# Performance work log

Hardware: AMD Instinct MI355X
Metric: run time of the kernel (lower is better)

The kernel has to match this reference:

```python
import math
import jax, jax.numpy as jnp
import numpy as np

N, D = 16384, 1024


def setup_inputs() -> dict:
    key = jax.random.key(0)
    k1, k2 = jax.random.split(key)
    return {
        "image_embeddings_aligned": jax.random.normal(k1, (N, D), dtype=jnp.float32),
        "text_embeddings_aligned": jax.random.normal(k2, (N, D), dtype=jnp.float32),
        "logit_scale": jnp.asarray(math.log(20.0), dtype=jnp.float32),  # stored as log(init)
        "logit_bias": jnp.asarray(-10.0, dtype=jnp.float32),
    }


def _l2_normalize(x, eps=1e-12):
    # matches F.normalize(p=2, dim=-1)
    n = jnp.linalg.norm(x, axis=-1, keepdims=True)
    return x / jnp.maximum(n, eps)


def reference(image_embeddings_aligned, text_embeddings_aligned, logit_scale, logit_bias):
    img = _l2_normalize(image_embeddings_aligned)
    txt = _l2_normalize(text_embeddings_aligned)
    # [N, N] pairwise logits
    logits = jnp.exp(logit_scale) * jnp.einsum("nd,md->nm", img, txt) + logit_bias
    n = logits.shape[0]
    labels = 2.0 * jnp.eye(n, dtype=logits.dtype) - 1.0  # +1 on diagonal, -1 off
    loss_matrix = jax.nn.log_sigmoid(labels * logits)
    siglip_loss = -jnp.mean(loss_matrix)  # total_loss (structure_lambda == 0)
    return siglip_loss
```

## Files before the change

### kernel.cpp

```cpp
#include <hip/hip_runtime.h>

#define NROWS 16384
#define DIM   1024
#define QSCALE 32.0f
#define E8M0S  0x7A7A7A7Au

typedef int    v4i    __attribute__((ext_vector_type(4)));
typedef int    v8i    __attribute__((ext_vector_type(8)));
typedef float  f32x16 __attribute__((ext_vector_type(16)));

__device__ __forceinline__ void glds16(const void* g, void* l) {
    __builtin_amdgcn_global_load_lds(
        (const __attribute__((address_space(1))) void*)g,
        (__attribute__((address_space(3))) void*)l,
        16, 0, 0);
}

__device__ __forceinline__ float fexp2(float x) {
#if __has_builtin(__builtin_amdgcn_exp2f)
    return __builtin_amdgcn_exp2f(x);
#else
    return exp2f(x);
#endif
}
__device__ __forceinline__ float flog2(float x) {
#if __has_builtin(__builtin_amdgcn_logf)
    return __builtin_amdgcn_logf(x);
#else
    return log2f(x);
#endif
}

__device__ __forceinline__ unsigned fp4_nib(float y) {
    unsigned s = (__float_as_uint(y) >> 31) << 3;
    float a = fminf(fabsf(y), 6.0f);
    unsigned c = (unsigned)(a >= 0.25f) + (unsigned)(a >= 0.75f) +
                 (unsigned)(a >= 1.25f) + (unsigned)(a >= 1.75f) +
                 (unsigned)(a >= 2.5f)  + (unsigned)(a >= 3.5f)  +
                 (unsigned)(a >= 5.0f);
    return c | s;
}

__global__ __launch_bounds__(256) void norm_fused(
    const float* __restrict__ img,
    const float* __restrict__ txt,
    unsigned char* __restrict__ imgQ,
    unsigned char* __restrict__ txtQ,
    const float* __restrict__ lscale,
    const float* __restrict__ lbias,
    float* __restrict__ diagPart) {
    const int t    = threadIdx.x;
    const int lane = t & 63;
    const int wave = t >> 6;
    const int gw   = blockIdx.x * 4 + wave;
    const float sc   = __expf(lscale[0]);
    const float bias = lbias[0];

    for (int row = gw; row < NROWS; row += 8192) {
        const float4* pi = (const float4*)(img + (size_t)row * DIM);
        const float4* pt = (const float4*)(txt + (size_t)row * DIM);
        float4 vi[4], vt[4];
        float ssi = 0.0f, sst = 0.0f, dot = 0.0f;
        #pragma unroll
        for (int j = 0; j < 4; ++j) {
            vi[j] = pi[lane * 4 + j];
            vt[j] = pt[lane * 4 + j];
            ssi += vi[j].x*vi[j].x + vi[j].y*vi[j].y + vi[j].z*vi[j].z + vi[j].w*vi[j].w;
            sst += vt[j].x*vt[j].x + vt[j].y*vt[j].y + vt[j].z*vt[j].z + vt[j].w*vt[j].w;
            dot += vi[j].x*vt[j].x + vi[j].y*vt[j].y + vi[j].z*vt[j].z + vi[j].w*vt[j].w;
        }
        #pragma unroll
        for (int off = 1; off < 64; off <<= 1) {
            ssi += __shfl_xor(ssi, off, 64);
            sst += __shfl_xor(sst, off, 64);
            dot += __shfl_xor(dot, off, 64);
        }
        const float ii = 1.0f / fmaxf(sqrtf(ssi), 1e-12f);
        const float it = 1.0f / fmaxf(sqrtf(sst), 1e-12f);
        if (lane == 0) diagPart[row] = -fmaf(sc, dot * ii * it, bias);

        const float qi = ii * QSCALE, qt = it * QSCALE;
        uint2 oi, ot;
        {
            const float* fi = (const float*)vi;
            const float* ft = (const float*)vt;
            unsigned lo = 0, hi = 0, lo2 = 0, hi2 = 0;
            #pragma unroll
            for (int e = 0; e < 8; ++e) {
                lo  |= fp4_nib(fi[e]     * qi) << (4 * e);
                hi  |= fp4_nib(fi[e + 8] * qi) << (4 * e);
                lo2 |= fp4_nib(ft[e]     * qt) << (4 * e);
                hi2 |= fp4_nib(ft[e + 8] * qt) << (4 * e);
            }
            oi.x = lo;  oi.y = hi;
            ot.x = lo2; ot.y = hi2;
        }
        ((uint2*)(imgQ + (size_t)row * 512))[lane] = oi;
        ((uint2*)(txtQ + (size_t)row * 512))[lane] = ot;
    }
}

__global__ __launch_bounds__(256) void siglip_gemm(
    const unsigned char* __restrict__ A,
    const unsigned char* __restrict__ B,
    const float* __restrict__ lscale,
    const float* __restrict__ lbias,
    float* __restrict__ gemmPart)
{
    __shared__ unsigned char sA[128 * 128];
    __shared__ unsigned char sB[128 * 128];
    __shared__ float wred[4];

    const int t    = threadIdx.x;
    const int lane = t & 63;
    const int wave = t >> 6;
    const int wr   = wave >> 1;
    const int wc   = wave & 1;
    const int r31  = lane & 31;
    const int h    = lane >> 5;
    const int xr   = (r31 & 7) ^ ((r31 >> 4) & 1);

    const int GRID = NROWS / 128;
    const int GM = 16;
    int b = blockIdx.x;
    int group = b / (GM * GRID);
    int ing   = b % (GM * GRID);
    int brow  = group * GM + (ing % GM);
    int bcol  = ing / GM;

    const size_t aBase = (size_t)brow * 128;
    const size_t bBase = (size_t)bcol * 128;

    const int srow = lane >> 3;
    const int c0   = (lane & 7) ^ srow;
    const int d01  = (c0 & 1) ? -16 : 16;

    const unsigned char* aP = A + (size_t)(aBase + wave * 32 + srow) * 512 + c0 * 16;
    const unsigned char* bP = B + (size_t)(bBase + wave * 32 + srow) * 512 + c0 * 16;
    char* lA0 = ((char*)sA) + wave * 4096;
    char* lB0 = ((char*)sB) + wave * 4096;

    int rbA[2], rbB[2];
    #pragma unroll
    for (int i = 0; i < 2; ++i) {
        rbA[i] = (wr * 64 + i * 32 + r31) * 128;
        rbB[i] = (wc * 64 + i * 32 + r31) * 128;
    }

    f32x16 acc[2][2] = {};

    for (int k = 0; k < 4; ++k) {
        __syncthreads();
        #pragma unroll
        for (int j = 0; j < 4; ++j) {
            const int tog = (j >> 1) ? d01 : 0;
            glds16(aP + j * 4096 + tog, lA0 + j * 1024);
            glds16(bP + j * 4096 + tog, lB0 + j * 1024);
        }
        aP += 128;
        bP += 128;
        __syncthreads();

        #pragma unroll
        for (int ks = 0; ks < 4; ++ks) {
            const int s = ((ks * 2 + h) ^ xr) * 16;
            v4i a0 = *(const v4i*)(sA + rbA[0] + s);
            v4i a1 = *(const v4i*)(sA + rbA[1] + s);
            v4i b0 = *(const v4i*)(sB + rbB[0] + s);
            v4i b1 = *(const v4i*)(sB + rbB[1] + s);
            v8i af[2], bf[2];
            af[0] = __builtin_shufflevector(a0, a0, 0, 1, 2, 3, -1, -1, -1, -1);
            af[1] = __builtin_shufflevector(a1, a1, 0, 1, 2, 3, -1, -1, -1, -1);
            bf[0] = __builtin_shufflevector(b0, b0, 0, 1, 2, 3, -1, -1, -1, -1);
            bf[1] = __builtin_shufflevector(b1, b1, 0, 1, 2, 3, -1, -1, -1, -1);
            #pragma unroll
            for (int mi = 0; mi < 2; ++mi)
                #pragma unroll
                for (int ni = 0; ni < 2; ++ni)
                    acc[mi][ni] = __builtin_amdgcn_mfma_scale_f32_32x32x64_f8f6f4(
                        af[mi], bf[ni], acc[mi][ni],
                        4, 4,
                        0, (int)E8M0S,
                        0, (int)E8M0S);
        }
    }

    const float l2e   = 1.44269504088896341f;
    const float scale = __expf(lscale[0]);
    const float aCo   = scale * l2e;
    const float bCo   = lbias[0] * l2e;
    float local = 0.0f;
    #pragma unroll
    for (int mi = 0; mi < 2; ++mi)
        #pragma unroll
        for (int ni = 0; ni < 2; ++ni)
            #pragma unroll
            for (int r = 0; r < 16; r += 4) {
                float e0 = fexp2(fmaf(aCo, acc[mi][ni][r + 0], bCo));
                float e1 = fexp2(fmaf(aCo, acc[mi][ni][r + 1], bCo));
                float e2 = fexp2(fmaf(aCo, acc[mi][ni][r + 2], bCo));
                float e3 = fexp2(fmaf(aCo, acc[mi][ni][r + 3], bCo));
                float p  = ((1.0f + e0) * (1.0f + e1)) *
                           ((1.0f + e2) * (1.0f + e3));
                local += flog2(p);
            }

    #pragma unroll
    for (int off = 32; off > 0; off >>= 1) local += __shfl_down(local, off, 64);
    if (lane == 0) wred[wave] = local;
    __syncthreads();
    if (t == 0)
        gemmPart[blockIdx.x] =
            (wred[0] + wred[1] + wred[2] + wred[3]) * 0.69314718055994531f;
}

__global__ __launch_bounds__(1024) void finalize_kernel(
    const float* __restrict__ parts, float* __restrict__ out) {
    __shared__ float wr[16];
    const int t    = threadIdx.x;
    const int lane = t & 63;
    const int wave = t >> 6;
    const float4* p4 = (const float4*)parts;
    float s = 0.0f;
    for (int i = t; i < 8192; i += 1024) {
        float4 v = p4[i];
        s += v.x + v.y + v.z + v.w;
    }
    #pragma unroll
    for (int off = 32; off > 0; off >>= 1) s += __shfl_down(s, off, 64);
    if (lane == 0) wr[wave] = s;
    __syncthreads();
    if (t == 0) {
        float tot = 0.0f;
        #pragma unroll
        for (int i = 0; i < 16; ++i) tot += wr[i];
        out[0] = tot / 268435456.0f;
    }
}

extern "C" void kernel_launch(void* const* d_in, const int* in_sizes, int n_in,
                              void* d_out, int out_size, void* d_ws, size_t ws_size,
                              hipStream_t stream) {
    const float* img    = (const float*)d_in[0];
    const float* txt    = (const float*)d_in[1];
    const float* lscale = (const float*)d_in[2];
    const float* lbias  = (const float*)d_in[3];
    float* out = (float*)d_out;

    char* ws = (char*)d_ws;
    unsigned char* imgQ = (unsigned char*)ws;
    unsigned char* txtQ = (unsigned char*)(ws + (size_t)NROWS * 512);
    float* parts   = (float*)(ws + (size_t)2 * NROWS * 512);
    float* diagPart = parts;
    float* gemmPart = parts + NROWS;

    norm_fused<<<2048, 256, 0, stream>>>(img, txt, imgQ, txtQ, lscale, lbias, diagPart);
    siglip_gemm<<<dim3((NROWS / 128) * (NROWS / 128)), 256, 0, stream>>>(
        imgQ, txtQ, lscale, lbias, gemmPart);
    finalize_kernel<<<1, 1024, 0, stream>>>(parts, out);
}
```

Measured before the change: 311.9 us.

## Enlarge GEMM tile to 256x128 and coalesce quantization loads/stores

```diff
diff --git a/kernel.cpp b/kernel.cpp
--- a/kernel.cpp
+++ b/kernel.cpp
@@ -63,8 +63,8 @@
         float ssi = 0.0f, sst = 0.0f, dot = 0.0f;
         #pragma unroll
         for (int j = 0; j < 4; ++j) {
-            vi[j] = pi[lane * 4 + j];
-            vt[j] = pt[lane * 4 + j];
+            vi[j] = pi[lane + 64 * j];
+            vt[j] = pt[lane + 64 * j];
             ssi += vi[j].x*vi[j].x + vi[j].y*vi[j].y + vi[j].z*vi[j].z + vi[j].w*vi[j].w;
             sst += vt[j].x*vt[j].x + vt[j].y*vt[j].y + vt[j].z*vt[j].z + vt[j].w*vt[j].w;
             dot += vi[j].x*vt[j].x + vi[j].y*vt[j].y + vi[j].z*vt[j].z + vi[j].w*vt[j].w;
@@ -80,34 +80,28 @@
         if (lane == 0) diagPart[row] = -fmaf(sc, dot * ii * it, bias);
 
         const float qi = ii * QSCALE, qt = it * QSCALE;
-        uint2 oi, ot;
-        {
-            const float* fi = (const float*)vi;
-            const float* ft = (const float*)vt;
-            unsigned lo = 0, hi = 0, lo2 = 0, hi2 = 0;
-            #pragma unroll
-            for (int e = 0; e < 8; ++e) {
-                lo  |= fp4_nib(fi[e]     * qi) << (4 * e);
-                hi  |= fp4_nib(fi[e + 8] * qi) << (4 * e);
-                lo2 |= fp4_nib(ft[e]     * qt) << (4 * e);
-                hi2 |= fp4_nib(ft[e + 8] * qt) << (4 * e);
-            }
-            oi.x = lo;  oi.y = hi;
-            ot.x = lo2; ot.y = hi2;
-        }
-        ((uint2*)(imgQ + (size_t)row * 512))[lane] = oi;
-        ((uint2*)(txtQ + (size_t)row * 512))[lane] = ot;
-    }
-}
-
-__global__ __launch_bounds__(256) void siglip_gemm(
+        ushort* oi = (ushort*)(imgQ + (size_t)row * 512);
+        ushort* ot = (ushort*)(txtQ + (size_t)row * 512);
+        #pragma unroll
+        for (int j = 0; j < 4; ++j) {
+            unsigned p = fp4_nib(vi[j].x * qi)        | (fp4_nib(vi[j].y * qi) << 4) |
+                         (fp4_nib(vi[j].z * qi) << 8) | (fp4_nib(vi[j].w * qi) << 12);
+            unsigned q = fp4_nib(vt[j].x * qt)        | (fp4_nib(vt[j].y * qt) << 4) |
+                         (fp4_nib(vt[j].z * qt) << 8) | (fp4_nib(vt[j].w * qt) << 12);
+            oi[lane + 64 * j] = (ushort)p;
+            ot[lane + 64 * j] = (ushort)q;
+        }
+    }
+}
+
+__global__ __launch_bounds__(256, 2) void siglip_gemm(
     const unsigned char* __restrict__ A,
     const unsigned char* __restrict__ B,
     const float* __restrict__ lscale,
     const float* __restrict__ lbias,
     float* __restrict__ gemmPart)
 {
-    __shared__ unsigned char sA[128 * 128];
+    __shared__ unsigned char sA[256 * 128];
     __shared__ unsigned char sB[128 * 128];
     __shared__ float wred[4];
 
@@ -120,42 +114,45 @@
     const int h    = lane >> 5;
     const int xr   = (r31 & 7) ^ ((r31 >> 4) & 1);
 
-    const int GRID = NROWS / 128;
+    const int GRID_N = NROWS / 128;
     const int GM = 16;
     int b = blockIdx.x;
-    int group = b / (GM * GRID);
-    int ing   = b % (GM * GRID);
+    int group = b / (GM * GRID_N);
+    int ing   = b % (GM * GRID_N);
     int brow  = group * GM + (ing % GM);
     int bcol  = ing / GM;
 
-    const size_t aBase = (size_t)brow * 128;
+    const size_t aBase = (size_t)brow * 256;
     const size_t bBase = (size_t)bcol * 128;
 
     const int srow = lane >> 3;
     const int c0   = (lane & 7) ^ srow;
     const int d01  = (c0 & 1) ? -16 : 16;
 
-    const unsigned char* aP = A + (size_t)(aBase + wave * 32 + srow) * 512 + c0 * 16;
+    const unsigned char* aP = A + (size_t)(aBase + wave * 64 + srow) * 512 + c0 * 16;
     const unsigned char* bP = B + (size_t)(bBase + wave * 32 + srow) * 512 + c0 * 16;
-    char* lA0 = ((char*)sA) + wave * 4096;
+    char* lA0 = ((char*)sA) + wave * 8192;
     char* lB0 = ((char*)sB) + wave * 4096;
 
-    int rbA[2], rbB[2];
-    #pragma unroll
-    for (int i = 0; i < 2; ++i) {
-        rbA[i] = (wr * 64 + i * 32 + r31) * 128;
-        rbB[i] = (wc * 64 + i * 32 + r31) * 128;
-    }
-
-    f32x16 acc[2][2] = {};
+    int rbA[4], rbB[2];
+    #pragma unroll
+    for (int i = 0; i < 4; ++i) rbA[i] = (wr * 128 + i * 32 + r31) * 128;
+    #pragma unroll
+    for (int i = 0; i < 2; ++i) rbB[i] = (wc * 64 + i * 32 + r31) * 128;
+
+    f32x16 acc[4][2] = {};
 
     for (int k = 0; k < 4; ++k) {
         __syncthreads();
         #pragma unroll
+        for (int j = 0; j < 8; ++j) {
+            const int tog = ((j >> 1) & 1) ? d01 : 0;
+            glds16(aP + j * 8 * 512 + tog, lA0 + j * 1024);
+        }
+        #pragma unroll
         for (int j = 0; j < 4; ++j) {
-            const int tog = (j >> 1) ? d01 : 0;
-            glds16(aP + j * 4096 + tog, lA0 + j * 1024);
-            glds16(bP + j * 4096 + tog, lB0 + j * 1024);
+            const int tog = ((j >> 1) & 1) ? d01 : 0;
+            glds16(bP + j * 8 * 512 + tog, lB0 + j * 1024);
         }
         aP += 128;
         bP += 128;
@@ -164,17 +161,19 @@
         #pragma unroll
         for (int ks = 0; ks < 4; ++ks) {
             const int s = ((ks * 2 + h) ^ xr) * 16;
-            v4i a0 = *(const v4i*)(sA + rbA[0] + s);
-            v4i a1 = *(const v4i*)(sA + rbA[1] + s);
-            v4i b0 = *(const v4i*)(sB + rbB[0] + s);
-            v4i b1 = *(const v4i*)(sB + rbB[1] + s);
-            v8i af[2], bf[2];
-            af[0] = __builtin_shufflevector(a0, a0, 0, 1, 2, 3, -1, -1, -1, -1);
-            af[1] = __builtin_shufflevector(a1, a1, 0, 1, 2, 3, -1, -1, -1, -1);
-            bf[0] = __builtin_shufflevector(b0, b0, 0, 1, 2, 3, -1, -1, -1, -1);
-            bf[1] = __builtin_shufflevector(b1, b1, 0, 1, 2, 3, -1, -1, -1, -1);
-            #pragma unroll
-            for (int mi = 0; mi < 2; ++mi)
+            v8i af[4], bf[2];
+            #pragma unroll
+            for (int i = 0; i < 4; ++i) {
+                v4i v = *(const v4i*)(sA + rbA[i] + s);
+                af[i] = __builtin_shufflevector(v, v, 0, 1, 2, 3, -1, -1, -1, -1);
+            }
+            #pragma unroll
+            for (int i = 0; i < 2; ++i) {
+                v4i v = *(const v4i*)(sB + rbB[i] + s);
+                bf[i] = __builtin_shufflevector(v, v, 0, 1, 2, 3, -1, -1, -1, -1);
+            }
+            #pragma unroll
+            for (int mi = 0; mi < 4; ++mi)
                 #pragma unroll
                 for (int ni = 0; ni < 2; ++ni)
                     acc[mi][ni] = __builtin_amdgcn_mfma_scale_f32_32x32x64_f8f6f4(
@@ -191,7 +190,7 @@
     const float bCo   = lbias[0] * l2e;
     float local = 0.0f;
     #pragma unroll
-    for (int mi = 0; mi < 2; ++mi)
+    for (int mi = 0; mi < 4; ++mi)
         #pragma unroll
         for (int ni = 0; ni < 2; ++ni)
             #pragma unroll
@@ -222,7 +221,7 @@
     const int wave = t >> 6;
     const float4* p4 = (const float4*)parts;
     float s = 0.0f;
-    for (int i = t; i < 8192; i += 1024) {
+    for (int i = t; i < 6144; i += 1024) {
         float4 v = p4[i];
         s += v.x + v.y + v.z + v.w;
     }
@@ -255,7 +254,7 @@
     float* gemmPart = parts + NROWS;
 
     norm_fused<<<2048, 256, 0, stream>>>(img, txt, imgQ, txtQ, lscale, lbias, diagPart);
-    siglip_gemm<<<dim3((NROWS / 128) * (NROWS / 128)), 256, 0, stream>>>(
+    siglip_gemm<<<dim3((NROWS / 256) * (NROWS / 128)), 256, 0, stream>>>(
         imgQ, txtQ, lscale, lbias, gemmPart);
     finalize_kernel<<<1, 1024, 0, stream>>>(parts, out);
 }
```

Result: no change. 310.0 us (-0.6%).
